# Kernel tuning notes

Hardware: AMD Instinct MI355X
Metric: run time of the kernel (lower is better)

Reference implementation:

```python
import jax, jax.numpy as jnp
import numpy as np
import math

PS = 8          # patch_size
OUT_C = 16      # out_channels
D_MODEL = 64
P_STATE = 32
BANDLIMIT = 1.0
STEP_SCALE = 1.0  # dt1 reference rate


def _ln(x, g, b, eps=1e-5):
    mu = jnp.mean(x, -1, keepdims=True)
    var = jnp.mean((x - mu) ** 2, -1, keepdims=True)
    return (x - mu) * jax.lax.rsqrt(var + eps) * g + b


def _forward(x, W_embed, b_embed, g1, beta1, Lambda_re, Lambda_im, B_re, B_im,
             C_re, C_im, D, log_step, g2, beta2, W_enc, W_dec, g3, beta3, W_out, b_out):
    b, t, h, w = x.shape
    hp, wp = h // PS, w // PS
    n = hp * wp
    # patchify: [b,t,h,w] -> [b,t,n,ps*ps]
    xp = x.reshape(b, t, hp, PS, wp, PS).transpose(0, 1, 2, 4, 3, 5).reshape(b, t, n, PS * PS)
    xe = xp @ W_embed.T + b_embed                              # [b,t,n,d]
    u = xe.transpose(0, 2, 1, 3).reshape(b * n, t, D_MODEL)    # [(b n), t, d]

    # ---- S5Block: pre-norm -> diagonal SSM -> gelu + residual -> GEGLU FFN ----
    fx = _ln(u, g1, beta1)
    Lam = Lambda_re + 1j * Lambda_im                           # [P] complex eigenvalues
    step = STEP_SCALE * jnp.exp(log_step)                      # [P]
    Lbar = jnp.exp(Lam * step)                                 # ZOH: A_bar
    Bbar = ((Lbar - 1.0) / Lam)[:, None] * (B_re + 1j * B_im)  # ZOH: B_bar [P,d]
    # bandlimit mask on C (freqs = step*|Im(Lambda)|/(2pi) < bandlimit/2)
    freqs = step * jnp.abs(Lambda_im) / (2.0 * math.pi)
    mask = (freqs < BANDLIMIT * 0.5).astype(C_re.dtype)
    Cc = (C_re + 1j * C_im) * mask[None, :]                    # [d,P]

    Bu = jnp.einsum('ntd,pd->ntp', fx.astype(jnp.complex64), Bbar)   # [(bn),t,P]
    A = jnp.broadcast_to(Lbar.astype(jnp.complex64), (1, t, P_STATE))

    def comb(e1, e2):
        a1, b1 = e1
        a2, b2 = e2
        return a1 * a2, a2 * b1 + b2

    _, xs = jax.lax.associative_scan(comb, (A, Bu), axis=1)    # x_k = A*x_{k-1} + Bu_k (x_0 = 0)
    ys = jnp.einsum('ntp,dp->ntd', xs, Cc).real + fx * D       # y = Re(C x) + D u
    xb = jax.nn.gelu(ys, approximate=False) + fx

    fx2 = _ln(xb, g2, beta2)
    enc = fx2 @ W_enc.T                                        # [(bn),t,2d]
    a, gate = jnp.split(enc, 2, axis=-1)
    xb = (a * jax.nn.gelu(gate, approximate=False)) @ W_dec.T + fx2

    # ---- take last timestep, project, unpatchify ----
    x_last = xb[:, -1, :]                                      # [(bn), d]
    proj = _ln(x_last, g3, beta3) @ W_out.T + b_out            # [(bn), C*ps*ps]
    y = proj.reshape(b, hp, wp, OUT_C, PS, PS).transpose(0, 3, 1, 4, 2, 5).reshape(b, OUT_C, h, w)
    return y


def setup_inputs() -> dict:
    key = jax.random.key(0)
    ks = jax.random.split(key, 12)
    d, P, pp = D_MODEL, P_STATE, PS * PS
    return dict(
        x=jax.random.normal(ks[0], (8, 15, 480, 640), jnp.float32),
        W_embed=jax.random.normal(ks[1], (d, pp), jnp.float32) / math.sqrt(pp),
        b_embed=jnp.zeros((d,), jnp.float32),
        g1=jnp.ones((d,), jnp.float32), beta1=jnp.zeros((d,), jnp.float32),
        Lambda_re=-0.5 * jnp.ones((P,), jnp.float32),
        Lambda_im=math.pi * (1.0 + jnp.arange(P, dtype=jnp.float32)),
        B_re=jax.random.normal(ks[2], (P, d), jnp.float32) / math.sqrt(d),
        B_im=jax.random.normal(ks[3], (P, d), jnp.float32) / math.sqrt(d),
        C_re=jax.random.normal(ks[4], (d, P), jnp.float32) / math.sqrt(P),
        C_im=jax.random.normal(ks[5], (d, P), jnp.float32) / math.sqrt(P),
        D=jax.random.normal(ks[6], (d,), jnp.float32),
        log_step=jax.random.uniform(ks[7], (P,), jnp.float32, math.log(1e-3), math.log(1e-1)),
        g2=jnp.ones((d,), jnp.float32), beta2=jnp.zeros((d,), jnp.float32),
        W_enc=jax.random.normal(ks[8], (2 * d, d), jnp.float32) / math.sqrt(d),
        W_dec=jax.random.normal(ks[9], (d, d), jnp.float32) / math.sqrt(d),
        g3=jnp.ones((d,), jnp.float32), beta3=jnp.zeros((d,), jnp.float32),
        W_out=jax.random.normal(ks[10], (OUT_C * pp, d), jnp.float32) / math.sqrt(d),
        b_out=jnp.zeros((OUT_C * pp,), jnp.float32),
    )


def reference(x, W_embed, b_embed, g1, beta1, Lambda_re, Lambda_im, B_re, B_im,
              C_re, C_im, D, log_step, g2, beta2, W_enc, W_dec, g3, beta3, W_out, b_out):
    return _forward(x, W_embed, b_embed, g1, beta1, Lambda_re, Lambda_im, B_re, B_im,
                    C_re, C_im, D, log_step, g2, beta2, W_enc, W_dec, g3, beta3, W_out, b_out)
```

## Files before the change

### kernel.cpp

```cpp
#include <hip/hip_runtime.h>
#include <math.h>


typedef __attribute__((ext_vector_type(8))) short short8;
typedef __attribute__((ext_vector_type(4))) float f32x4;

#define MFMA16(a, b, c) __builtin_amdgcn_mfma_f32_16x16x32_bf16((a), (b), (c), 0, 0, 0)

__device__ __forceinline__ short f2bf(float f) {
  union { float f; unsigned u; } v; v.f = f;
  unsigned r = (v.u + 0x7fffu + ((v.u >> 16) & 1u)) >> 16;
  return (short)r;
}
__device__ __forceinline__ float geluf(float x) {
  return 0.5f * x * (1.0f + erff(x * 0.70710678118654752f));
}
__device__ __forceinline__ short8 packfrag(const f32x4& a, const f32x4& b) {
  short8 o;
  o[0] = f2bf(a[0]); o[1] = f2bf(a[1]); o[2] = f2bf(a[2]); o[3] = f2bf(a[3]);
  o[4] = f2bf(b[0]); o[5] = f2bf(b[1]); o[6] = f2bf(b[2]); o[7] = f2bf(b[3]);
  return o;
}
__device__ __forceinline__ int ecmap(int i, int m) {
  return (i >> 1) * 32 + (m >> 2) * 8 + (i & 1) * 4 + (m & 3);
}
__device__ __forceinline__ void bbar_factors(const float* Lre, const float* Lim,
                                             const float* lstep, int p,
                                             float& fre, float& fim) {
  float st = expf(lstep[p]);
  float lr = Lre[p], li = Lim[p];
  float er = expf(lr * st);
  float lbr = er * cosf(li * st), lbi = er * sinf(li * st);
  float u = lbr - 1.0f, v = lbi;
  float den = lr * lr + li * li;
  fre = (u * lr + v * li) / den;
  fim = (v * lr - u * li) / den;
}

__global__ __launch_bounds__(256) void k0_prep(
    const float* __restrict__ W_embed, const float* __restrict__ g1,
    const float* __restrict__ be1, const float* __restrict__ Lre,
    const float* __restrict__ Lim, const float* __restrict__ Bre,
    const float* __restrict__ Bim, const float* __restrict__ Cre,
    const float* __restrict__ Cim, const float* __restrict__ lstep,
    const float* __restrict__ W_enc, const float* __restrict__ W_dec,
    const float* __restrict__ W_out, short* __restrict__ wimg,
    float* __restrict__ bu0) {
  const int bid = blockIdx.x;
  if (bid == 44) {
    int q = threadIdx.x;
    if (q < 64) {
      int c = q >> 5, p = q & 31;
      float fre, fim; bbar_factors(Lre, Lim, lstep, p, fre, fim);
      float s = 0.f;
      for (int d = 0; d < 64; ++d) {
        float br = Bre[p * 64 + d], bi = Bim[p * 64 + d];
        float val = c ? (fre * bi + fim * br) : (fre * br - fim * bi);
        s += be1[d] * val;
      }
      bu0[q] = s;
    }
    return;
  }
  const int w = threadIdx.x >> 6, lane = threadIdx.x & 63;
  const int m = lane & 15, qd = lane >> 4;
  const int f = bid * 4 + w;
  short v[8];
  if (f < 8) {
    int i = f >> 1, kt = f & 1, chan = ecmap(i, m), k0 = kt * 32 + qd * 8;
#pragma unroll
    for (int j = 0; j < 8; ++j) v[j] = f2bf(W_embed[chan * 64 + k0 + j]);
  } else if (f < 16) {
    int fi = f - 8, i = fi >> 1, kt = fi & 1;
    int comp = i & 1, p = (i >> 1) * 16 + m, d0 = kt * 32 + qd * 8;
    float fre, fim; bbar_factors(Lre, Lim, lstep, p, fre, fim);
#pragma unroll
    for (int j = 0; j < 8; ++j) {
      int d = d0 + j;
      float br = Bre[p * 64 + d], bi = Bim[p * 64 + d];
      float val = comp ? (fre * bi + fim * br) : (fre * br - fim * bi);
      v[j] = f2bf(g1[d] * val);
    }
  } else if (f < 24) {
    int fi = f - 16, i = fi >> 1, kt = fi & 1, chan = ecmap(i, m);
#pragma unroll
    for (int j = 0; j < 8; ++j) {
      int comp = j >> 2, p = kt * 16 + qd * 4 + (j & 3);
      float stp = expf(lstep[p]);
      float fr = stp * fabsf(Lim[p]) * (1.0f / 6.28318530717958648f);
      float msk = (fr < 0.5f) ? 1.f : 0.f;
      float val = comp ? -Cim[chan * 32 + p] * msk : Cre[chan * 32 + p] * msk;
      v[j] = f2bf(val);
    }
  } else if (f < 40) {
    int fi = f - 24, i = fi >> 1, kt = fi & 1;
    int row = (i < 4) ? ecmap(i, m) : 64 + ecmap(i - 4, m);
#pragma unroll
    for (int j = 0; j < 8; ++j) v[j] = f2bf(W_enc[row * 64 + kt * 32 + qd * 8 + j]);
  } else if (f < 48) {
    int fi = f - 40, i = fi >> 1, kt = fi & 1, row = ecmap(i, m);
#pragma unroll
    for (int j = 0; j < 8; ++j) v[j] = f2bf(W_dec[row * 64 + kt * 32 + qd * 8 + j]);
  } else {
    int fi = f - 48, i = fi >> 1, kt = fi & 1, row = i * 16 + m;
#pragma unroll
    for (int j = 0; j < 8; ++j) v[j] = f2bf(W_out[row * 64 + kt * 32 + qd * 8 + j]);
  }
  short8 sv;
#pragma unroll
  for (int j = 0; j < 8; ++j) sv[j] = v[j];
  *(short8*)&wimg[(f * 64 + lane) * 8] = sv;
}

__global__ __launch_bounds__(256) void k1_fused(
    const float* __restrict__ x, const short* __restrict__ wimg_g,
    const float* __restrict__ bu0_g, const float* __restrict__ Lre,
    const float* __restrict__ Lim, const float* __restrict__ lstep,
    const float* __restrict__ g1, const float* __restrict__ be1,
    const float* __restrict__ bemb, const float* __restrict__ Dv,
    const float* __restrict__ g2, const float* __restrict__ be2,
    float* __restrict__ xlastT) {
  __shared__ short wimg[48 * 512];
  {
    float4* dst = (float4*)wimg;
    const float4* src = (const float4*)wimg_g;
    for (int i = threadIdx.x; i < 3072; i += 256) dst[i] = src[i];
  }
  __syncthreads();
#define WF(id) (*(const short8*)&wimg[(id) * 512 + lane * 8])

  const int wv = threadIdx.x >> 6, lane = threadIdx.x & 63;
  const int s = lane & 15, qd = lane >> 4;
  const int sbase = (blockIdx.x * 4 + wv) * 16;
  const int b_i = sbase / 4800;
  const int pr = sbase % 4800;
  const int ph = pr / 80;
  const int pw0 = pr % 80;
  const float* xbase = x + ((b_i * 15) * 480 + ph * 8) * 640 + (pw0 + s) * 8;

  int cb[4];
  f32x4 bec[4], bu0c[4];
#pragma unroll
  for (int nt = 0; nt < 4; ++nt) {
    cb[nt] = (nt >> 1) * 32 + qd * 8 + (nt & 1) * 4;
    bec[nt] = *(const f32x4*)(bemb + cb[nt]);
    bu0c[nt] = *(const f32x4*)(bu0_g + (nt & 1) * 32 + (nt >> 1) * 16 + qd * 4);
  }
  f32x4 lbr[2], lbi[2];
#pragma unroll
  for (int k = 0; k < 2; ++k)
#pragma unroll
    for (int r = 0; r < 4; ++r) {
      int p = k * 16 + qd * 4 + r;
      float st = expf(lstep[p]);
      float er = expf(Lre[p] * st);
      lbr[k][r] = er * cosf(Lim[p] * st);
      lbi[k][r] = er * sinf(Lim[p] * st);
    }

  const f32x4 zf = {0.f, 0.f, 0.f, 0.f};
  f32x4 state[4] = {zf, zf, zf, zf};
  f32x4 xh[4];

  f32x4 vcur[4], vnext[4];
#pragma unroll
  for (int kt = 0; kt < 2; ++kt) {
    const float* rp = xbase + (kt * 4 + qd) * 640;
    vcur[kt * 2] = *(const f32x4*)rp;
    vcur[kt * 2 + 1] = *(const f32x4*)(rp + 4);
  }

  for (int t = 0; t < 15; ++t) {
    if (t < 14) {
      const float* xn = xbase + (t + 1) * 307200;
#pragma unroll
      for (int kt = 0; kt < 2; ++kt) {
        const float* rp = xn + (kt * 4 + qd) * 640;
        vnext[kt * 2] = *(const f32x4*)rp;
        vnext[kt * 2 + 1] = *(const f32x4*)(rp + 4);
      }
    }
    short8 pa0 = packfrag(vcur[0], vcur[1]);
    short8 pa1 = packfrag(vcur[2], vcur[3]);
    f32x4 c1[4];
#pragma unroll
    for (int i = 0; i < 4; ++i) {
      f32x4 acc = MFMA16(WF(i * 2), pa0, zf);
      acc = MFMA16(WF(i * 2 + 1), pa1, acc);
      c1[i] = acc + bec[i];
    }
    float sm = 0.f, sq = 0.f;
#pragma unroll
    for (int nt = 0; nt < 4; ++nt)
#pragma unroll
      for (int i = 0; i < 4; ++i) { sm += c1[nt][i]; sq += c1[nt][i] * c1[nt][i]; }
    sm += __shfl_xor(sm, 16); sq += __shfl_xor(sq, 16);
    sm += __shfl_xor(sm, 32); sq += __shfl_xor(sq, 32);
    float mean = sm * 0.015625f;
    float rstd = rsqrtf(sq * 0.015625f - mean * mean + 1e-5f);
#pragma unroll
    for (int nt = 0; nt < 4; ++nt) xh[nt] = (c1[nt] - mean) * rstd;
    short8 xa0 = packfrag(xh[0], xh[1]);
    short8 xa1 = packfrag(xh[2], xh[3]);
#pragma unroll
    for (int k = 0; k < 2; ++k) {
      f32x4 re = state[2 * k], im = state[2 * k + 1];
      state[2 * k]     = lbr[k] * re - lbi[k] * im + bu0c[2 * k];
      state[2 * k + 1] = lbr[k] * im + lbi[k] * re + bu0c[2 * k + 1];
    }
#pragma unroll
    for (int i = 0; i < 4; ++i) {
      state[i] = MFMA16(WF(8 + i * 2), xa0, state[i]);
      state[i] = MFMA16(WF(8 + i * 2 + 1), xa1, state[i]);
    }
#pragma unroll
    for (int q = 0; q < 4; ++q) vcur[q] = vnext[q];
  }

  f32x4 g1c[4], b1c[4], Dc[4], g2c[4], b2c[4];
#pragma unroll
  for (int nt = 0; nt < 4; ++nt) {
    g1c[nt] = *(const f32x4*)(g1 + cb[nt]);
    b1c[nt] = *(const f32x4*)(be1 + cb[nt]);
    Dc[nt] = *(const f32x4*)(Dv + cb[nt]);
    g2c[nt] = *(const f32x4*)(g2 + cb[nt]);
    b2c[nt] = *(const f32x4*)(be2 + cb[nt]);
  }
  f32x4 fxl[4];
#pragma unroll
  for (int nt = 0; nt < 4; ++nt) fxl[nt] = xh[nt] * g1c[nt] + b1c[nt];

  short8 xsa0 = packfrag(state[0], state[1]);
  short8 xsa1 = packfrag(state[2], state[3]);
  f32x4 xbv[4];
#pragma unroll
  for (int i = 0; i < 4; ++i) {
    f32x4 acc = fxl[i] * Dc[i];
    acc = MFMA16(WF(16 + i * 2), xsa0, acc);
    acc = MFMA16(WF(16 + i * 2 + 1), xsa1, acc);
#pragma unroll
    for (int r = 0; r < 4; ++r) xbv[i][r] = geluf(acc[r]) + fxl[i][r];
  }
  float sm2 = 0.f, sq2 = 0.f;
#pragma unroll
  for (int nt = 0; nt < 4; ++nt)
#pragma unroll
    for (int i = 0; i < 4; ++i) { sm2 += xbv[nt][i]; sq2 += xbv[nt][i] * xbv[nt][i]; }
  sm2 += __shfl_xor(sm2, 16); sq2 += __shfl_xor(sq2, 16);
  sm2 += __shfl_xor(sm2, 32); sq2 += __shfl_xor(sq2, 32);
  float mean2 = sm2 * 0.015625f;
  float rstd2 = rsqrtf(sq2 * 0.015625f - mean2 * mean2 + 1e-5f);
  f32x4 fx2[4];
#pragma unroll
  for (int nt = 0; nt < 4; ++nt)
    fx2[nt] = (xbv[nt] - mean2) * rstd2 * g2c[nt] + b2c[nt];

  short8 fa0 = packfrag(fx2[0], fx2[1]);
  short8 fa1 = packfrag(fx2[2], fx2[3]);
  f32x4 e[8];
#pragma unroll
  for (int i = 0; i < 8; ++i) {
    f32x4 acc = MFMA16(WF(24 + i * 2), fa0, zf);
    e[i] = MFMA16(WF(24 + i * 2 + 1), fa1, acc);
  }
  f32x4 hv[4];
#pragma unroll
  for (int nt = 0; nt < 4; ++nt)
#pragma unroll
    for (int i = 0; i < 4; ++i) hv[nt][i] = e[nt][i] * geluf(e[nt + 4][i]);

  short8 ha0 = packfrag(hv[0], hv[1]);
  short8 ha1 = packfrag(hv[2], hv[3]);
  f32x4 xo[4];
#pragma unroll
  for (int i = 0; i < 4; ++i) {
    f32x4 acc = fx2[i];
    acc = MFMA16(WF(40 + i * 2), ha0, acc);
    xo[i] = MFMA16(WF(40 + i * 2 + 1), ha1, acc);
  }
#pragma unroll
  for (int kt = 0; kt < 2; ++kt)
#pragma unroll
    for (int j = 0; j < 8; ++j)
      xlastT[(kt * 32 + qd * 8 + j) * 38400 + sbase + s] = xo[2 * kt + (j >> 2)][j & 3];
#undef WF
}

__global__ __launch_bounds__(256) void k2_head(
    const float* __restrict__ xlastT, const short* __restrict__ wout_img,
    const float* __restrict__ g3, const float* __restrict__ be3,
    const float* __restrict__ b_out, float* __restrict__ y) {
  __shared__ short wo[32 * 512];
  const int nqb = blockIdx.x & 3;
  const int mblk = blockIdx.x >> 2;
  {
    float4* dst = (float4*)wo;
    const float4* src = (const float4*)(wout_img + nqb * 32 * 512);
    for (int i = threadIdx.x; i < 2048; i += 256) dst[i] = src[i];
  }
  __syncthreads();
  const int wv = threadIdx.x >> 6, lane = threadIdx.x & 63;
  const int s = lane & 15, qd = lane >> 4;
  const int sbase = mblk * 64 + wv * 16;
  const int seq = sbase + s;
  const int nq0 = nqb * 256;

  float vals[2][8];
#pragma unroll
  for (int kt = 0; kt < 2; ++kt)
#pragma unroll
    for (int j = 0; j < 8; ++j)
      vals[kt][j] = xlastT[(kt * 32 + qd * 8 + j) * 38400 + seq];
  float sm = 0.f, sq = 0.f;
#pragma unroll
  for (int kt = 0; kt < 2; ++kt)
#pragma unroll
    for (int j = 0; j < 8; ++j) { sm += vals[kt][j]; sq += vals[kt][j] * vals[kt][j]; }
  sm += __shfl_xor(sm, 16); sq += __shfl_xor(sq, 16);
  sm += __shfl_xor(sm, 32); sq += __shfl_xor(sq, 32);
  float mean = sm * 0.015625f;
  float rstd = rsqrtf(sq * 0.015625f - mean * mean + 1e-5f);

  short8 zb[2];
#pragma unroll
  for (int kt = 0; kt < 2; ++kt) {
    f32x4 ga = *(const f32x4*)(g3 + kt * 32 + qd * 8);
    f32x4 gb = *(const f32x4*)(g3 + kt * 32 + qd * 8 + 4);
    f32x4 ba = *(const f32x4*)(be3 + kt * 32 + qd * 8);
    f32x4 bb = *(const f32x4*)(be3 + kt * 32 + qd * 8 + 4);
#pragma unroll
    for (int j = 0; j < 4; ++j) {
      zb[kt][j] = f2bf((vals[kt][j] - mean) * rstd * ga[j] + ba[j]);
      zb[kt][j + 4] = f2bf((vals[kt][j + 4] - mean) * rstd * gb[j] + bb[j]);
    }
  }
  const int bi2 = seq / 4800, prr = seq % 4800;
  const int phh = prr / 80, pww = prr % 80;
  const int obase = (bi2 * 16 * 480 + phh * 8) * 640 + pww * 8;

#pragma unroll
  for (int nt = 0; nt < 16; ++nt) {
    int o0 = nq0 + nt * 16 + qd * 4;
    f32x4 acc = *(const f32x4*)(b_out + o0);
    acc = MFMA16(*(const short8*)&wo[(nt * 2 + 0) * 512 + lane * 8], zb[0], acc);
    acc = MFMA16(*(const short8*)&wo[(nt * 2 + 1) * 512 + lane * 8], zb[1], acc);
    int c = o0 >> 6, pi = (o0 >> 3) & 7, pj = o0 & 7;
    *(f32x4*)&y[obase + c * 307200 + pi * 640 + pj] = acc;
  }
}

extern "C" void kernel_launch(void* const* d_in, const int* in_sizes, int n_in,
                              void* d_out, int out_size, void* d_ws, size_t ws_size,
                              hipStream_t stream) {
  const float* x       = (const float*)d_in[0];
  const float* W_embed = (const float*)d_in[1];
  const float* b_embed = (const float*)d_in[2];
  const float* g1      = (const float*)d_in[3];
  const float* beta1   = (const float*)d_in[4];
  const float* Lre     = (const float*)d_in[5];
  const float* Lim     = (const float*)d_in[6];
  const float* Bre     = (const float*)d_in[7];
  const float* Bim     = (const float*)d_in[8];
  const float* Cre     = (const float*)d_in[9];
  const float* Cim     = (const float*)d_in[10];
  const float* Dv      = (const float*)d_in[11];
  const float* lstep   = (const float*)d_in[12];
  const float* g2      = (const float*)d_in[13];
  const float* beta2   = (const float*)d_in[14];
  const float* W_enc   = (const float*)d_in[15];
  const float* W_dec   = (const float*)d_in[16];
  const float* g3      = (const float*)d_in[17];
  const float* beta3   = (const float*)d_in[18];
  const float* W_out   = (const float*)d_in[19];
  const float* b_out   = (const float*)d_in[20];
  float* y = (float*)d_out;

  short* wimg = (short*)d_ws;
  float* bu0 = (float*)((char*)d_ws + 176 * 1024);
  float* xlastT = (float*)((char*)d_ws + 180 * 1024);

  k0_prep<<<dim3(45), dim3(256), 0, stream>>>(W_embed, g1, beta1, Lre, Lim,
                                              Bre, Bim, Cre, Cim, lstep,
                                              W_enc, W_dec, W_out, wimg, bu0);
  k1_fused<<<dim3(600), dim3(256), 0, stream>>>(x, wimg, bu0, Lre, Lim, lstep,
                                                g1, beta1, b_embed, Dv, g2,
                                                beta2, xlastT);
  k2_head<<<dim3(2400), dim3(256), 0, stream>>>(xlastT, wimg + 48 * 512, g3,
                                                beta3, b_out, y);
}
```

Measured before the change: 350.3 us.

## Stage input patches through swizzled double-buffered LDS with coalesced loads

Each block now loads its input patches with coalesced float4 reads and stages them into a swizzled, double-buffered shared-memory tile. Loads are issued two timesteps ahead and each wave reads its MFMA fragments from LDS. Previously every lane fetched strided rows straight from global memory. Only the first 16 weight fragments are kept in LDS during the time loop, and the rest are reloaded into the freed buffer space afterwards, so shared memory fits in 48KB. Launch bounds now request 3 blocks per CU. The cost is extra block-wide barriers every timestep and possible register pressure from the staging registers.

Result: slower. 442.5 us (+26.3%).

```diff
diff --git a/kernel.cpp b/kernel.cpp
--- a/kernel.cpp
+++ b/kernel.cpp
@@ -23,6 +23,9 @@
 }
 __device__ __forceinline__ int ecmap(int i, int m) {
   return (i >> 1) * 32 + (m >> 2) * 8 + (i & 1) * 4 + (m & 3);
+}
+__device__ __forceinline__ int swz(int b) {
+  return b ^ (((b >> 2) ^ (b >> 6)) & 0x60) ^ (((b >> 3) ^ (b >> 9)) & 0x10);
 }
 __device__ __forceinline__ void bbar_factors(const float* Lre, const float* Lim,
                                              const float* lstep, int p,
@@ -112,7 +115,7 @@
   *(short8*)&wimg[(f * 64 + lane) * 8] = sv;
 }
 
-__global__ __launch_bounds__(256) void k1_fused(
+__global__ __launch_bounds__(256, 3) void k1_fused(
     const float* __restrict__ x, const short* __restrict__ wimg_g,
     const float* __restrict__ bu0_g, const float* __restrict__ Lre,
     const float* __restrict__ Lim, const float* __restrict__ lstep,
@@ -120,23 +123,41 @@
     const float* __restrict__ bemb, const float* __restrict__ Dv,
     const float* __restrict__ g2, const float* __restrict__ be2,
     float* __restrict__ xlastT) {
-  __shared__ short wimg[48 * 512];
+  __shared__ __align__(16) char smem[49152];
+#define WF(id) (*(const short8*)(smem + (id) * 1024 + lane * 16))
+
+  const int tid = threadIdx.x;
+  const int wv = tid >> 6, lane = tid & 63;
+  const int s = lane & 15, qd = lane >> 4;
+
+  float4 wreg[4];
   {
-    float4* dst = (float4*)wimg;
     const float4* src = (const float4*)wimg_g;
-    for (int i = threadIdx.x; i < 3072; i += 256) dst[i] = src[i];
-  }
-  __syncthreads();
-#define WF(id) (*(const short8*)&wimg[(id) * 512 + lane * 8])
-
-  const int wv = threadIdx.x >> 6, lane = threadIdx.x & 63;
-  const int s = lane & 15, qd = lane >> 4;
+#pragma unroll
+    for (int j = 0; j < 4; ++j) wreg[j] = src[j * 256 + tid];
+  }
+
+  int off[4], slot[4];
+#pragma unroll
+  for (int j = 0; j < 4; ++j) {
+    int c = j * 256 + tid;
+    int r = c >> 7, p = (c >> 1) & 63, h = c & 1;
+    int seq = blockIdx.x * 64 + p;
+    int b_i = seq / 4800, pr = seq % 4800;
+    int ph = pr / 80, pw = pr % 80;
+    off[j] = ((b_i * 15) * 480 + ph * 8 + r) * 640 + pw * 8 + h * 4;
+    slot[j] = swz(c * 16);
+  }
+  int rb[4];
+#pragma unroll
+  for (int kt = 0; kt < 2; ++kt)
+#pragma unroll
+    for (int h = 0; h < 2; ++h) {
+      int b = (kt * 4 + qd) * 2048 + (wv * 16 + s) * 32 + h * 16;
+      rb[kt * 2 + h] = swz(b);
+    }
+
   const int sbase = (blockIdx.x * 4 + wv) * 16;
-  const int b_i = sbase / 4800;
-  const int pr = sbase % 4800;
-  const int ph = pr / 80;
-  const int pw0 = pr % 80;
-  const float* xbase = x + ((b_i * 15) * 480 + ph * 8) * 640 + (pw0 + s) * 8;
 
   int cb[4];
   f32x4 bec[4], bu0c[4];
@@ -158,28 +179,37 @@
       lbi[k][r] = er * sinf(Lim[p] * st);
     }
 
+  float4 stg0[4], stgA[4];
+#pragma unroll
+  for (int j = 0; j < 4; ++j) stg0[j] = *(const float4*)(x + off[j]);
+#pragma unroll
+  for (int j = 0; j < 4; ++j) stgA[j] = *(const float4*)(x + off[j] + 307200);
+  {
+    float4* wdst = (float4*)smem;
+#pragma unroll
+    for (int j = 0; j < 4; ++j) wdst[j * 256 + tid] = wreg[j];
+    char* b0 = smem + 16384;
+#pragma unroll
+    for (int j = 0; j < 4; ++j) *(float4*)(b0 + slot[j]) = stg0[j];
+  }
+  __syncthreads();
+
   const f32x4 zf = {0.f, 0.f, 0.f, 0.f};
   f32x4 state[4] = {zf, zf, zf, zf};
   f32x4 xh[4];
-
-  f32x4 vcur[4], vnext[4];
-#pragma unroll
-  for (int kt = 0; kt < 2; ++kt) {
-    const float* rp = xbase + (kt * 4 + qd) * 640;
-    vcur[kt * 2] = *(const f32x4*)rp;
-    vcur[kt * 2 + 1] = *(const f32x4*)(rp + 4);
-  }
+  f32x4 vcur[4];
 
   for (int t = 0; t < 15; ++t) {
-    if (t < 14) {
-      const float* xn = xbase + (t + 1) * 307200;
-#pragma unroll
-      for (int kt = 0; kt < 2; ++kt) {
-        const float* rp = xn + (kt * 4 + qd) * 640;
-        vnext[kt * 2] = *(const f32x4*)rp;
-        vnext[kt * 2 + 1] = *(const f32x4*)(rp + 4);
-      }
-    }
+    float4 stgB[4];
+    if (t < 13) {
+#pragma unroll
+      for (int j = 0; j < 4; ++j)
+        stgB[j] = *(const float4*)(x + off[j] + (t + 2) * 307200);
+    }
+    const char* bufr = smem + 16384 + ((t & 1) << 14);
+#pragma unroll
+    for (int q = 0; q < 4; ++q) vcur[q] = *(const f32x4*)(bufr + rb[q]);
+
     short8 pa0 = packfrag(vcur[0], vcur[1]);
     short8 pa1 = packfrag(vcur[2], vcur[3]);
     f32x4 c1[4];
@@ -213,9 +243,31 @@
       state[i] = MFMA16(WF(8 + i * 2), xa0, state[i]);
       state[i] = MFMA16(WF(8 + i * 2 + 1), xa1, state[i]);
     }
-#pragma unroll
-    for (int q = 0; q < 4; ++q) vcur[q] = vnext[q];
-  }
+
+    if (t < 14) {
+      __syncthreads();
+      char* bufw = smem + 16384 + (((t + 1) & 1) << 14);
+#pragma unroll
+      for (int j = 0; j < 4; ++j) *(float4*)(bufw + slot[j]) = stgA[j];
+      __syncthreads();
+      if (t < 13) {
+#pragma unroll
+        for (int j = 0; j < 4; ++j) stgA[j] = stgB[j];
+      }
+    }
+  }
+
+  __syncthreads();
+  {
+    float4 hf[8];
+    const float4* src = (const float4*)(wimg_g + 16 * 512);
+#pragma unroll
+    for (int j = 0; j < 8; ++j) hf[j] = src[j * 256 + tid];
+    float4* dst = (float4*)(smem + 16384);
+#pragma unroll
+    for (int j = 0; j < 8; ++j) dst[j * 256 + tid] = hf[j];
+  }
+  __syncthreads();
 
   f32x4 g1c[4], b1c[4], Dc[4], g2c[4], b2c[4];
 #pragma unroll
```
